# Kernel tuning notes

Measured on AMD Instinct MI355X. Metric: run time of the kernel, lower is better.

## Reference

```python
import jax, jax.numpy as jnp
import numpy as np

EPS = 1e-8
TEMPERATURE = 0.5


def setup_inputs() -> dict:
    key = jax.random.key(0)
    k1, k2, k3, k4 = jax.random.split(key, 4)
    B, DIN, DOUT = 4096, 2048, 128
    return {
        "zi": jax.random.normal(k1, (B, DIN), dtype=jnp.float32),
        "zj": jax.random.normal(k2, (B, DIN), dtype=jnp.float32),
        "W": jax.random.normal(k3, (DOUT, DIN), dtype=jnp.float32) * 0.02,
        "b": jax.random.normal(k4, (DOUT,), dtype=jnp.float32) * 0.02,
    }


def reference(zi, zj, W, b):
    # MLP projection head: Linear(ReLU(x))
    hi = jax.nn.relu(zi) @ W.T + b  # [B, 128]
    hj = jax.nn.relu(zj) @ W.T + b  # [B, 128]
    B = hi.shape[0]
    N = 2 * B
    reps = jnp.concatenate([hi, hj], axis=0)  # [2B, 128]
    # Cosine similarity: normalize once (torch eps=1e-8 clamp), then one matmul
    norms = jnp.maximum(jnp.linalg.norm(reps, axis=-1, keepdims=True), EPS)
    zn = reps / norms
    sim = (zn @ zn.T) / TEMPERATURE  # [2B, 2B]
    idx = jnp.arange(N)
    # positive pair index: i <-> i +/- B
    pos = sim[idx, (idx + B) % N]  # [2B]
    # denominator: all j != i (self excluded, positive included once) ==
    # torch's [positive, negatives(mask excludes diag and +/-B diags)] logits
    NEG_INF = jnp.asarray(-1e9, sim.dtype)
    sim_masked = jnp.where(idx[:, None] == idx[None, :], NEG_INF, sim)
    lse = jax.scipy.special.logsumexp(sim_masked, axis=1)  # [2B]
    loss = jnp.mean(lse - pos)
    return loss
```

## Files before the change

### kernel.cpp

```cpp
#include <hip/hip_runtime.h>
#include <math.h>

#define DIN    2048
#define DOUT   128
#define BHALF  4096
#define NTOT   8192
#define NSPLIT 8
#define JSPAN  1024

typedef __bf16 bf16x8 __attribute__((ext_vector_type(8)));
typedef float  f32x4  __attribute__((ext_vector_type(4)));
typedef unsigned int u32x4 __attribute__((ext_vector_type(4)));

#define MFMA16 __builtin_amdgcn_mfma_f32_16x16x32_bf16

struct PackedPair { unsigned int h, l; };

__device__ __forceinline__ unsigned int bf16_rne(float f) {
    unsigned int u = __float_as_uint(f);
    return (u + 0x7fffu + ((u >> 16) & 1u)) >> 16;
}
__device__ __forceinline__ float bf16f(unsigned int h) {
    return __uint_as_float(h << 16);
}
__device__ __forceinline__ PackedPair split2(float a, float b) {
    unsigned int h0 = bf16_rne(a), h1 = bf16_rne(b);
    unsigned int g0 = bf16_rne(a - bf16f(h0)), g1 = bf16_rne(b - bf16f(h1));
    PackedPair r;
    r.h = h0 | (h1 << 16);
    r.l = g0 | (g1 << 16);
    return r;
}


__global__ __launch_bounds__(256) void wsplit_kernel(
    const float* __restrict__ W,
    unsigned short* __restrict__ Whp, unsigned short* __restrict__ Wlp,
    float* __restrict__ out)
{
    int t = blockIdx.x * 256 + threadIdx.x;
    if (t == 0) out[0] = 0.f;
    int l  = t & 63;
    int ks = (t >> 6) & 63;
    int g  = t >> 12;
    int c  = g * 16 + (l & 15);
    int k0 = ks * 32 + ((l >> 4) << 3);
    const float* src = W + (size_t)c * DIN + k0;
    f32x4 v0 = *(const f32x4*)src;
    f32x4 v1 = *(const f32x4*)(src + 4);
    u32x4 hv, lv;
    PackedPair p0 = split2(v0[0], v0[1]);  hv[0] = p0.h; lv[0] = p0.l;
    PackedPair p1 = split2(v0[2], v0[3]);  hv[1] = p1.h; lv[1] = p1.l;
    PackedPair p2 = split2(v1[0], v1[1]);  hv[2] = p2.h; lv[2] = p2.l;
    PackedPair p3 = split2(v1[2], v1[3]);  hv[3] = p3.h; lv[3] = p3.l;
    size_t off = ((size_t)(g * 64 + ks) * 64 + l) * 8;
    *(u32x4*)(Whp + off) = hv;
    *(u32x4*)(Wlp + off) = lv;
}

__global__ __launch_bounds__(512) void proj_kernel(
    const float* __restrict__ zi, const float* __restrict__ zj,
    const unsigned short* __restrict__ Whp, const unsigned short* __restrict__ Wlp,
    const float* __restrict__ bvec,
    unsigned short* __restrict__ Zhp, unsigned short* __restrict__ Zlp)
{
    __shared__ float Red[4][32][128];
    const int t = threadIdx.x;
    const int w = t >> 6;
    const int lane = t & 63;
    const int r15 = lane & 15, q = lane >> 4;
    const int row0 = blockIdx.x * 32;
    const float* zsrc = (row0 < BHALF) ? zi : zj;
    const int zr0 = (row0 < BHALF) ? row0 : row0 - BHALF;

    f32x4 acc[2][8];
    #pragma unroll
    for (int m = 0; m < 2; m++)
        #pragma unroll
        for (int g = 0; g < 8; g++) acc[m][g] = (f32x4){0.f, 0.f, 0.f, 0.f};

    for (int ks = w * 8; ks < w * 8 + 8; ks++) {
        const int k0 = ks * 32 + q * 8;
        bf16x8 ah[2], al[2];
        #pragma unroll
        for (int m = 0; m < 2; m++) {
            const float* s = zsrc + (size_t)(zr0 + m * 16 + r15) * DIN + k0;
            f32x4 v0 = *(const f32x4*)s;
            f32x4 v1 = *(const f32x4*)(s + 4);
            #pragma unroll
            for (int p = 0; p < 4; p++) {
                v0[p] = fmaxf(v0[p], 0.f);
                v1[p] = fmaxf(v1[p], 0.f);
            }
            u32x4 hv, lv;
            PackedPair p0 = split2(v0[0], v0[1]);  hv[0] = p0.h; lv[0] = p0.l;
            PackedPair p1 = split2(v0[2], v0[3]);  hv[1] = p1.h; lv[1] = p1.l;
            PackedPair p2 = split2(v1[0], v1[1]);  hv[2] = p2.h; lv[2] = p2.l;
            PackedPair p3 = split2(v1[2], v1[3]);  hv[3] = p3.h; lv[3] = p3.l;
            ah[m] = __builtin_bit_cast(bf16x8, hv);
            al[m] = __builtin_bit_cast(bf16x8, lv);
        }
        #pragma unroll
        for (int g = 0; g < 8; g++) {
            size_t bo = ((size_t)(g * 64 + ks) * 64 + lane) * 8;
            bf16x8 bh = __builtin_bit_cast(bf16x8, *(const u32x4*)(Whp + bo));
            bf16x8 bl = __builtin_bit_cast(bf16x8, *(const u32x4*)(Wlp + bo));
            #pragma unroll
            for (int m = 0; m < 2; m++) {
                acc[m][g] = MFMA16(ah[m], bh, acc[m][g], 0, 0, 0);
                acc[m][g] = MFMA16(ah[m], bl, acc[m][g], 0, 0, 0);
                acc[m][g] = MFMA16(al[m], bh, acc[m][g], 0, 0, 0);
            }
        }
    }

    if (w >= 4) {
        #pragma unroll
        for (int m = 0; m < 2; m++)
            #pragma unroll
            for (int g = 0; g < 8; g++)
                #pragma unroll
                for (int r = 0; r < 4; r++)
                    Red[w - 4][m * 16 + q * 4 + r][g * 16 + r15] = acc[m][g][r];
    }
    __syncthreads();
    if (w < 4) {
        #pragma unroll
        for (int m = 0; m < 2; m++)
            #pragma unroll
            for (int g = 0; g < 8; g++)
                #pragma unroll
                for (int r = 0; r < 4; r++) {
                    int rr = m * 16 + q * 4 + r, cc = g * 16 + r15;
                    Red[w][rr][cc] += acc[m][g][r];
                }
    }
    __syncthreads();

    const int ty = t >> 5;
    const int tx = t & 31;
    const f32x4 bb = *(const f32x4*)(bvec + tx * 4);
    #pragma unroll
    for (int i = 0; i < 2; i++) {
        const int row = ty * 2 + i;
        f32x4 v = (f32x4){0.f, 0.f, 0.f, 0.f};
        #pragma unroll
        for (int ww = 0; ww < 4; ww++)
            v += *(const f32x4*)&Red[ww][row][tx * 4];
        v += bb;
        float ssq = v[0]*v[0] + v[1]*v[1] + v[2]*v[2] + v[3]*v[3];
        #pragma unroll
        for (int msk = 1; msk < 32; msk <<= 1) ssq += __shfl_xor(ssq, msk);
        const float inv = 1.f / fmaxf(sqrtf(ssq), 1e-8f);
        const int grow = row0 + row;
        const int gg = grow >> 4, rr = grow & 15;
        #pragma unroll
        for (int j = 0; j < 4; j++) {
            const int k = tx * 4 + j;
            float x = v[j] * inv;
            unsigned int h  = bf16_rne(x);
            unsigned int lo = bf16_rne(x - bf16f(h));
            size_t off = (((size_t)gg * 4 + (k >> 5)) * 64
                          + (rr | (((k >> 3) & 3) << 4))) * 8 + (k & 7);
            Zhp[off] = (unsigned short)h;
            Zlp[off] = (unsigned short)lo;
        }
    }
}

__global__ __launch_bounds__(256) void sim_kernel(
    const unsigned short* __restrict__ Zhp, const unsigned short* __restrict__ Zlp,
    float* __restrict__ Spart, float* __restrict__ P)
{
    __shared__ unsigned short Jt[16384];
    const int t = threadIdx.x;
    const int w = t >> 6, lane = t & 63;
    const int r15 = lane & 15, rq = lane >> 4;
    const int iblk   = blockIdx.x >> 3;
    const int jsplit = blockIdx.x & 7;
    const int rowbase = iblk * 128 + w * 32;

    bf16x8 Ah[2][4], Al[2][4];
    #pragma unroll
    for (int m = 0; m < 2; m++) {
        const int gA = iblk * 8 + w * 2 + m;
        #pragma unroll
        for (int ks = 0; ks < 4; ks++) {
            size_t ao = (((size_t)gA * 4 + ks) * 64 + lane) * 8;
            Ah[m][ks] = __builtin_bit_cast(bf16x8, *(const u32x4*)(Zhp + ao));
            Al[m][ks] = __builtin_bit_cast(bf16x8, *(const u32x4*)(Zlp + ao));
        }
    }

    float rs[2][4], ps[2][4];
    #pragma unroll
    for (int m = 0; m < 2; m++)
        #pragma unroll
        for (int r = 0; r < 4; r++) { rs[m][r] = 0.f; ps[m][r] = 0.f; }

    for (int jt = 0; jt < JSPAN / 64; jt++) {
        const int j0 = jsplit * JSPAN + jt * 64;
        __syncthreads();
        #pragma unroll
        for (int rr = 0; rr < 8; rr++) {
            int flat = t + rr * 256;
            int cid = flat >> 6, ll = flat & 63;
            int hl = cid >> 4, jg = (cid >> 2) & 3, ks = cid & 3;
            const unsigned short* src = hl ? Zlp : Zhp;
            size_t so = (((size_t)((j0 >> 4) + jg) * 4 + ks) * 64 + ll) * 8;
            *(u32x4*)&Jt[(size_t)flat * 8] = *(const u32x4*)(src + so);
        }
        __syncthreads();

        f32x4 acc[2][4];
        #pragma unroll
        for (int m = 0; m < 2; m++)
            #pragma unroll
            for (int jg = 0; jg < 4; jg++) acc[m][jg] = (f32x4){0.f,0.f,0.f,0.f};

        #pragma unroll
        for (int ks = 0; ks < 4; ks++) {
            #pragma unroll
            for (int jg = 0; jg < 4; jg++) {
                bf16x8 bh = __builtin_bit_cast(bf16x8,
                    *(const u32x4*)&Jt[((jg * 4 + ks) * 64 + lane) * 8]);
                bf16x8 bl = __builtin_bit_cast(bf16x8,
                    *(const u32x4*)&Jt[((jg * 4 + ks + 16) * 64 + lane) * 8]);
                #pragma unroll
                for (int m = 0; m < 2; m++) {
                    acc[m][jg] = MFMA16(Ah[m][ks], bh, acc[m][jg], 0, 0, 0);
                    acc[m][jg] = MFMA16(Ah[m][ks], bl, acc[m][jg], 0, 0, 0);
                    acc[m][jg] = MFMA16(Al[m][ks], bh, acc[m][jg], 0, 0, 0);
                }
            }
        }

        #pragma unroll
        for (int m = 0; m < 2; m++) {
            const int growb = rowbase + m * 16 + rq * 4;
            #pragma unroll
            for (int jg = 0; jg < 4; jg++) {
                const int gcol = j0 + jg * 16 + r15;
                #pragma unroll
                for (int r = 0; r < 4; r++) {
                    float s = 2.f * acc[m][jg][r];
                    const int grow = growb + r;
                    float e = __expf(s);
                    if (gcol == grow) e = 0.f;
                    rs[m][r] += e;
                    if (gcol == (grow ^ BHALF)) ps[m][r] += s;
                }
            }
        }
    }

    #pragma unroll
    for (int m = 0; m < 2; m++)
        #pragma unroll
        for (int r = 0; r < 4; r++) {
            float a = rs[m][r], p = ps[m][r];
            #pragma unroll
            for (int msk = 1; msk < 16; msk <<= 1) {
                a += __shfl_xor(a, msk);
                p += __shfl_xor(p, msk);
            }
            if (r15 == 0) {
                const int grow = rowbase + m * 16 + rq * 4 + r;
                Spart[jsplit * NTOT + grow] = a;
                if (((grow ^ BHALF) >> 10) == jsplit) P[grow] = p;
            }
        }
}

__global__ __launch_bounds__(256) void loss_kernel(
    const float* __restrict__ Spart, const float* __restrict__ P,
    float* __restrict__ out)
{
    const int i = blockIdx.x * 256 + threadIdx.x;
    float ssum = 0.f;
    #pragma unroll
    for (int sp = 0; sp < NSPLIT; sp++) ssum += Spart[sp * NTOT + i];
    float v = logf(ssum) - P[i];
    #pragma unroll
    for (int msk = 1; msk < 64; msk <<= 1) v += __shfl_xor(v, msk);
    __shared__ float red[4];
    if ((threadIdx.x & 63) == 0) red[threadIdx.x >> 6] = v;
    __syncthreads();
    if (threadIdx.x == 0)
        atomicAdd(out, (red[0] + red[1] + red[2] + red[3]) * (1.f / (float)NTOT));
}

extern "C" void kernel_launch(void* const* d_in, const int* in_sizes, int n_in,
                              void* d_out, int out_size, void* d_ws, size_t ws_size,
                              hipStream_t stream) {
    const float* zi = (const float*)d_in[0];
    const float* zj = (const float*)d_in[1];
    const float* W  = (const float*)d_in[2];
    const float* bv = (const float*)d_in[3];
    float* out = (float*)d_out;

    char* ws = (char*)d_ws;
    unsigned short* Whp = (unsigned short*)(ws);
    unsigned short* Wlp = (unsigned short*)(ws + (512 << 10));
    unsigned short* Zhp = (unsigned short*)(ws + (1024 << 10));
    unsigned short* Zlp = (unsigned short*)(ws + (3072 << 10));
    float* Spart = (float*)(ws);
    float* P     = (float*)(ws + (256 << 10));

    wsplit_kernel<<<128, 256, 0, stream>>>(W, Whp, Wlp, out);
    proj_kernel<<<256, 512, 0, stream>>>(zi, zj, Whp, Wlp, bv, Zhp, Zlp);
    sim_kernel<<<512, 256, 0, stream>>>(Zhp, Zlp, Spart, P);
    loss_kernel<<<NTOT / 256, 256, 0, stream>>>(Spart, P, out);
}
```

Baseline: 189.5 us.

## Halve per-block rows in proj and split sim j-range 16 ways with direct LDS loads

The projection kernel now handles 16 rows per block instead of 32, doubling the grid. It software-prefetches the next z chunk in registers, pads the reduction buffer to reduce bank conflicts, and adds an occupancy hint. The similarity kernel splits the column range into 16 parts instead of 8, doubling its grid, and stages tiles with global_load_lds instead of going through registers. These changes aim to fill more CUs and hide load latency, at the cost of re-reading W twice as often, more partial sums, and a loss kernel that still sums only NSPLIT partials.

Measured after the change: 198.5 us. 1.05x slower.

```diff
diff --git a/kernel.cpp b/kernel.cpp
--- a/kernel.cpp
+++ b/kernel.cpp
@@ -5,8 +5,8 @@
 #define DOUT   128
 #define BHALF  4096
 #define NTOT   8192
-#define NSPLIT 8
-#define JSPAN  1024
+#define NSPLIT 16
+#define JSPAN  512
 
 typedef __bf16 bf16x8 __attribute__((ext_vector_type(8)));
 typedef float  f32x4  __attribute__((ext_vector_type(4)));
@@ -58,117 +58,107 @@
     *(u32x4*)(Wlp + off) = lv;
 }
 
-__global__ __launch_bounds__(512) void proj_kernel(
+__global__ __launch_bounds__(512, 4) void proj_kernel(
     const float* __restrict__ zi, const float* __restrict__ zj,
     const unsigned short* __restrict__ Whp, const unsigned short* __restrict__ Wlp,
     const float* __restrict__ bvec,
     unsigned short* __restrict__ Zhp, unsigned short* __restrict__ Zlp)
 {
-    __shared__ float Red[4][32][128];
+    __shared__ float Red[4][16][132];
     const int t = threadIdx.x;
     const int w = t >> 6;
     const int lane = t & 63;
     const int r15 = lane & 15, q = lane >> 4;
-    const int row0 = blockIdx.x * 32;
+    const int row0 = blockIdx.x * 16;
     const float* zsrc = (row0 < BHALF) ? zi : zj;
     const int zr0 = (row0 < BHALF) ? row0 : row0 - BHALF;
 
-    f32x4 acc[2][8];
-    #pragma unroll
-    for (int m = 0; m < 2; m++)
-        #pragma unroll
-        for (int g = 0; g < 8; g++) acc[m][g] = (f32x4){0.f, 0.f, 0.f, 0.f};
-
-    for (int ks = w * 8; ks < w * 8 + 8; ks++) {
-        const int k0 = ks * 32 + q * 8;
-        bf16x8 ah[2], al[2];
-        #pragma unroll
-        for (int m = 0; m < 2; m++) {
-            const float* s = zsrc + (size_t)(zr0 + m * 16 + r15) * DIN + k0;
-            f32x4 v0 = *(const f32x4*)s;
-            f32x4 v1 = *(const f32x4*)(s + 4);
-            #pragma unroll
-            for (int p = 0; p < 4; p++) {
-                v0[p] = fmaxf(v0[p], 0.f);
-                v1[p] = fmaxf(v1[p], 0.f);
-            }
-            u32x4 hv, lv;
-            PackedPair p0 = split2(v0[0], v0[1]);  hv[0] = p0.h; lv[0] = p0.l;
-            PackedPair p1 = split2(v0[2], v0[3]);  hv[1] = p1.h; lv[1] = p1.l;
-            PackedPair p2 = split2(v1[0], v1[1]);  hv[2] = p2.h; lv[2] = p2.l;
-            PackedPair p3 = split2(v1[2], v1[3]);  hv[3] = p3.h; lv[3] = p3.l;
-            ah[m] = __builtin_bit_cast(bf16x8, hv);
-            al[m] = __builtin_bit_cast(bf16x8, lv);
-        }
+    f32x4 acc[8];
+    #pragma unroll
+    for (int g = 0; g < 8; g++) acc[g] = (f32x4){0.f, 0.f, 0.f, 0.f};
+
+    const float* zrow = zsrc + (size_t)(zr0 + r15) * DIN + q * 8;
+    f32x4 pv0 = *(const f32x4*)(zrow + w * 256);
+    f32x4 pv1 = *(const f32x4*)(zrow + w * 256 + 4);
+
+    #pragma unroll
+    for (int i = 0; i < 8; i++) {
+        const int ks = w * 8 + i;
+        f32x4 v0 = pv0, v1 = pv1;
+        if (i < 7) {
+            pv0 = *(const f32x4*)(zrow + w * 256 + (i + 1) * 32);
+            pv1 = *(const f32x4*)(zrow + w * 256 + (i + 1) * 32 + 4);
+        }
+        #pragma unroll
+        for (int p = 0; p < 4; p++) {
+            v0[p] = fmaxf(v0[p], 0.f);
+            v1[p] = fmaxf(v1[p], 0.f);
+        }
+        u32x4 hv, lv;
+        PackedPair p0 = split2(v0[0], v0[1]);  hv[0] = p0.h; lv[0] = p0.l;
+        PackedPair p1 = split2(v0[2], v0[3]);  hv[1] = p1.h; lv[1] = p1.l;
+        PackedPair p2 = split2(v1[0], v1[1]);  hv[2] = p2.h; lv[2] = p2.l;
+        PackedPair p3 = split2(v1[2], v1[3]);  hv[3] = p3.h; lv[3] = p3.l;
+        bf16x8 ah = __builtin_bit_cast(bf16x8, hv);
+        bf16x8 al = __builtin_bit_cast(bf16x8, lv);
         #pragma unroll
         for (int g = 0; g < 8; g++) {
             size_t bo = ((size_t)(g * 64 + ks) * 64 + lane) * 8;
             bf16x8 bh = __builtin_bit_cast(bf16x8, *(const u32x4*)(Whp + bo));
             bf16x8 bl = __builtin_bit_cast(bf16x8, *(const u32x4*)(Wlp + bo));
-            #pragma unroll
-            for (int m = 0; m < 2; m++) {
-                acc[m][g] = MFMA16(ah[m], bh, acc[m][g], 0, 0, 0);
-                acc[m][g] = MFMA16(ah[m], bl, acc[m][g], 0, 0, 0);
-                acc[m][g] = MFMA16(al[m], bh, acc[m][g], 0, 0, 0);
-            }
+            acc[g] = MFMA16(ah, bh, acc[g], 0, 0, 0);
+            acc[g] = MFMA16(ah, bl, acc[g], 0, 0, 0);
+            acc[g] = MFMA16(al, bh, acc[g], 0, 0, 0);
         }
     }
 
     if (w >= 4) {
         #pragma unroll
-        for (int m = 0; m < 2; m++)
-            #pragma unroll
-            for (int g = 0; g < 8; g++)
-                #pragma unroll
-                for (int r = 0; r < 4; r++)
-                    Red[w - 4][m * 16 + q * 4 + r][g * 16 + r15] = acc[m][g][r];
+        for (int g = 0; g < 8; g++)
+            #pragma unroll
+            for (int r = 0; r < 4; r++)
+                Red[w - 4][q * 4 + r][g * 16 + r15] = acc[g][r];
     }
     __syncthreads();
     if (w < 4) {
         #pragma unroll
-        for (int m = 0; m < 2; m++)
-            #pragma unroll
-            for (int g = 0; g < 8; g++)
-                #pragma unroll
-                for (int r = 0; r < 4; r++) {
-                    int rr = m * 16 + q * 4 + r, cc = g * 16 + r15;
-                    Red[w][rr][cc] += acc[m][g][r];
-                }
+        for (int g = 0; g < 8; g++)
+            #pragma unroll
+            for (int r = 0; r < 4; r++)
+                Red[w][q * 4 + r][g * 16 + r15] += acc[g][r];
     }
     __syncthreads();
 
-    const int ty = t >> 5;
-    const int tx = t & 31;
+    const int row = t >> 5;
+    const int tx  = t & 31;
+    float v[4];
+    #pragma unroll
+    for (int j = 0; j < 4; j++) {
+        v[j] = Red[0][row][tx * 4 + j] + Red[1][row][tx * 4 + j]
+             + Red[2][row][tx * 4 + j] + Red[3][row][tx * 4 + j];
+    }
     const f32x4 bb = *(const f32x4*)(bvec + tx * 4);
-    #pragma unroll
-    for (int i = 0; i < 2; i++) {
-        const int row = ty * 2 + i;
-        f32x4 v = (f32x4){0.f, 0.f, 0.f, 0.f};
-        #pragma unroll
-        for (int ww = 0; ww < 4; ww++)
-            v += *(const f32x4*)&Red[ww][row][tx * 4];
-        v += bb;
-        float ssq = v[0]*v[0] + v[1]*v[1] + v[2]*v[2] + v[3]*v[3];
-        #pragma unroll
-        for (int msk = 1; msk < 32; msk <<= 1) ssq += __shfl_xor(ssq, msk);
-        const float inv = 1.f / fmaxf(sqrtf(ssq), 1e-8f);
-        const int grow = row0 + row;
-        const int gg = grow >> 4, rr = grow & 15;
-        #pragma unroll
-        for (int j = 0; j < 4; j++) {
-            const int k = tx * 4 + j;
-            float x = v[j] * inv;
-            unsigned int h  = bf16_rne(x);
-            unsigned int lo = bf16_rne(x - bf16f(h));
-            size_t off = (((size_t)gg * 4 + (k >> 5)) * 64
-                          + (rr | (((k >> 3) & 3) << 4))) * 8 + (k & 7);
-            Zhp[off] = (unsigned short)h;
-            Zlp[off] = (unsigned short)lo;
-        }
-    }
-}
-
-__global__ __launch_bounds__(256) void sim_kernel(
+    v[0] += bb[0]; v[1] += bb[1]; v[2] += bb[2]; v[3] += bb[3];
+    float ssq = v[0]*v[0] + v[1]*v[1] + v[2]*v[2] + v[3]*v[3];
+    #pragma unroll
+    for (int msk = 1; msk < 32; msk <<= 1) ssq += __shfl_xor(ssq, msk);
+    const float inv = 1.f / fmaxf(sqrtf(ssq), 1e-8f);
+    const int grow = row0 + row;
+    const int gg = grow >> 4, rr = grow & 15;
+    #pragma unroll
+    for (int j = 0; j < 4; j++) {
+        const int k = tx * 4 + j;
+        float x = v[j] * inv;
+        unsigned int h  = bf16_rne(x);
+        unsigned int lo = bf16_rne(x - bf16f(h));
+        size_t off = (((size_t)gg * 4 + (k >> 5)) * 64
+                      + (rr | (((k >> 3) & 3) << 4))) * 8 + (k & 7);
+        Zhp[off] = (unsigned short)h;
+        Zlp[off] = (unsigned short)lo;
+    }
+}
+
+__global__ __launch_bounds__(256, 4) void sim_kernel(
     const unsigned short* __restrict__ Zhp, const unsigned short* __restrict__ Zlp,
     float* __restrict__ Spart, float* __restrict__ P)
 {
@@ -176,8 +166,8 @@
     const int t = threadIdx.x;
     const int w = t >> 6, lane = t & 63;
     const int r15 = lane & 15, rq = lane >> 4;
-    const int iblk   = blockIdx.x >> 3;
-    const int jsplit = blockIdx.x & 7;
+    const int iblk   = blockIdx.x >> 4;
+    const int jsplit = blockIdx.x & 15;
     const int rowbase = iblk * 128 + w * 32;
 
     bf16x8 Ah[2][4], Al[2][4];
@@ -203,12 +193,15 @@
         __syncthreads();
         #pragma unroll
         for (int rr = 0; rr < 8; rr++) {
-            int flat = t + rr * 256;
-            int cid = flat >> 6, ll = flat & 63;
-            int hl = cid >> 4, jg = (cid >> 2) & 3, ks = cid & 3;
+            const int cid = rr * 4 + w;
+            const int hl = cid >> 4, jg = (cid >> 2) & 3, ks = cid & 3;
             const unsigned short* src = hl ? Zlp : Zhp;
-            size_t so = (((size_t)((j0 >> 4) + jg) * 4 + ks) * 64 + ll) * 8;
-            *(u32x4*)&Jt[(size_t)flat * 8] = *(const u32x4*)(src + so);
+            const unsigned short* gp = src
+                + (((size_t)((j0 >> 4) + jg) * 4 + ks) * 64 + lane) * 8;
+            unsigned short* lp = &Jt[(size_t)(rr * 256 + w * 64) * 8];
+            __builtin_amdgcn_global_load_lds(
+                (const __attribute__((address_space(1))) unsigned int*)gp,
+                (__attribute__((address_space(3))) unsigned int*)lp, 16, 0, 0);
         }
         __syncthreads();
 
@@ -267,7 +260,7 @@
             if (r15 == 0) {
                 const int grow = rowbase + m * 16 + rq * 4 + r;
                 Spart[jsplit * NTOT + grow] = a;
-                if (((grow ^ BHALF) >> 10) == jsplit) P[grow] = p;
+                if (((grow ^ BHALF) >> 9) == jsplit) P[grow] = p;
             }
         }
 }
@@ -305,10 +298,10 @@
     unsigned short* Zhp = (unsigned short*)(ws + (1024 << 10));
     unsigned short* Zlp = (unsigned short*)(ws + (3072 << 10));
     float* Spart = (float*)(ws);
-    float* P     = (float*)(ws + (256 << 10));
+    float* P     = (float*)(ws + (512 << 10));
 
     wsplit_kernel<<<128, 256, 0, stream>>>(W, Whp, Wlp, out);
-    proj_kernel<<<256, 512, 0, stream>>>(zi, zj, Whp, Wlp, bv, Zhp, Zlp);
-    sim_kernel<<<512, 256, 0, stream>>>(Zhp, Zlp, Spart, P);
+    proj_kernel<<<512, 512, 0, stream>>>(zi, zj, Whp, Wlp, bv, Zhp, Zlp);
+    sim_kernel<<<1024, 256, 0, stream>>>(Zhp, Zlp, Spart, P);
     loss_kernel<<<NTOT / 256, 256, 0, stream>>>(Spart, P, out);
 }
```
